# Kernel optimization log

Hardware: AMD Instinct MI355X
Metric: run time of the kernel (lower is better)

Reference implementation:

```python
import jax, jax.numpy as jnp
import numpy as np

B, L, S = 32, 8192, 128  # E == S == D == 128 required by the einsum labeling

def setup_inputs() -> dict:
    key = jax.random.key(0)
    kq, kk, kv = jax.random.split(key, 3)
    queries = jax.random.normal(kq, (B, L, S), dtype=jnp.float32)
    keys = jax.random.normal(kk, (B, S, S), dtype=jnp.float32)
    values = jax.random.normal(kv, (B, S, S), dtype=jnp.float32)
    return {"queries": queries, "keys": keys, "values": values}

def reference(queries, keys, values):
    # queries: (B, L, E), keys/values: (B, S, D) with E == S == D.
    # scores_1: sum-pooled outer product term (reduced-rank additive score)
    s1 = queries.sum(-1)[:, :, None] * keys.sum(-1)[:, None, :]   # (B, L, S)
    # scores_2: q contracted against key-position axis (plain batched matmul, no transpose)
    s2 = jnp.einsum('bls,bsd->bld', queries, keys)                # (B, L, S)
    A = jax.nn.softmax(s1 + s2, axis=-1)                          # (B, L, S)
    out = jnp.einsum('bls,bsd->bld', A, values)                   # (B, L, D)
    # original returns shape (B, 1, L, D) for the 3D-input path
    return out[:, None, :, :]
```

## Files before the change

kernel.cpp:

```cpp
#include <hip/hip_runtime.h>

#define SDIM 128
#define LDIM 8192
#define BATCH 32

#define WS_BATCH_BYTES 98304

typedef __attribute__((ext_vector_type(8))) short short8;
typedef __attribute__((ext_vector_type(16))) float float16;

union S8U { short8 v; unsigned short u[8]; unsigned w[4]; };
union FU { float f; unsigned u; };

static __device__ __forceinline__ unsigned short f2bf(float x) {
    FU v; v.f = x;
    unsigned r = v.u + 0x7fffu + ((v.u >> 16) & 1u);
    return (unsigned short)(r >> 16);
}
static __device__ __forceinline__ float bf2f(unsigned short h) {
    FU v; v.u = ((unsigned)h) << 16; return v.f;
}
static __device__ __forceinline__ float16 mfma_bf16(short8 a, short8 b, float16 c) {
    return __builtin_amdgcn_mfma_f32_32x32x16_bf16(a, b, c, 0, 0, 0);
}

__global__ __launch_bounds__(256) void prep_kernel(
        const float* __restrict__ keys, const float* __restrict__ values,
        char* __restrict__ ws) {
    __shared__ float T[SDIM * SDIM];
    __shared__ float ksum_s[SDIM];
    const int blk = blockIdx.x;
    const int b = blk >> 2;
    const int which = (blk >> 1) & 1;
    const int half = blk & 1;
    const int tid = threadIdx.x;
    const float* src = (which ? values : keys) + (size_t)b * SDIM * SDIM;

    #pragma unroll
    for (int it = 0; it < 16; ++it) {
        int i = tid + it * 256;
        int r = i >> 5, c0 = (i & 31) * 4;
        float4 v = ((const float4*)src)[i];
        float f[4] = {v.x, v.y, v.z, v.w};
        #pragma unroll
        for (int k = 0; k < 4; ++k)
            T[r * SDIM + ((c0 + k + r) & 127)] = f[k];
    }
    __syncthreads();

    if (which == 0) {
        int row = tid >> 1, hf = tid & 1;
        float s = 0.f;
        #pragma unroll
        for (int i = 0; i < 64; ++i) s += T[row * SDIM + hf * 64 + i];
        s += __shfl_xor(s, 1, 64);
        if (hf == 0) ksum_s[row] = s;
    }
    __syncthreads();

    char* dst = ws + (size_t)b * WS_BATCH_BYTES + (which ? 65536 : 0);
    #pragma unroll
    for (int it = 0; it < 4; ++it) {
        int entry = half * 1024 + it * 256 + tid;
        int m = entry >> 9;
        int ks = (entry >> 6) & 7;
        int lane = entry & 63;
        int ln = lane & 31, H = lane >> 5;
        int r = 32 * m + ln;
        int c0 = 16 * ks + 8 * H;
        if (which == 0) {
            float add = ksum_s[r];
            S8U hi, lo;
            #pragma unroll
            for (int i = 0; i < 8; ++i) {
                int e = c0 + i;
                float x = T[e * SDIM + ((r + e) & 127)] + add;
                unsigned short h = f2bf(x);
                hi.u[i] = h;
                lo.u[i] = f2bf(x - bf2f(h));
            }
            *(short8*)(dst + entry * 16) = hi.v;
            *(short8*)(dst + 32768 + entry * 16) = lo.v;
        } else {
            S8U hv;
            #pragma unroll
            for (int i = 0; i < 8; ++i) {
                int j = c0 + i;
                hv.u[i] = f2bf(T[j * SDIM + ((r + j) & 127)]);
            }
            *(short8*)(dst + entry * 16) = hv.v;
        }
    }
}

__global__ __launch_bounds__(256, 2) void attn_kernel(
        const float* __restrict__ q, const char* __restrict__ ws,
        float* __restrict__ out) {
    __shared__ char smQ[65536];
    const int blk = blockIdx.x;
    const int b = blk >> 6, tile = blk & 63;
    const int tid = threadIdx.x, wave = tid >> 6, lane = tid & 63;
    const int H = lane >> 5, ln = lane & 31;

    const char* wsb = ws + (size_t)b * WS_BATCH_BYTES;
    const float* qblk = q + ((size_t)b * LDIM + tile * 128) * SDIM;
    float* ob = out + ((size_t)b * LDIM + tile * 128 + wave * 32) * SDIM;

    {
        float4 buf[8][2];
        #pragma unroll
        for (int it = 0; it < 8; ++it) {
            int idx = it * 256 + tid;
            const float* p = qblk + (idx >> 4) * SDIM + (idx & 15) * 8;
            buf[it][0] = *(const float4*)p;
            buf[it][1] = *(const float4*)(p + 4);
        }
        #pragma unroll
        for (int it = 0; it < 8; ++it) {
            int idx = it * 256 + tid;
            int row = idx >> 4, cc = idx & 15;
            float f[8] = {buf[it][0].x, buf[it][0].y, buf[it][0].z, buf[it][0].w,
                          buf[it][1].x, buf[it][1].y, buf[it][1].z, buf[it][1].w};
            unsigned hiw[4], low[4];
            #pragma unroll
            for (int pr = 0; pr < 4; ++pr) {
                FU u0, u1; u0.f = f[2 * pr]; u1.f = f[2 * pr + 1];
                unsigned r0 = u0.u + 0x7fffu + ((u0.u >> 16) & 1u);
                unsigned r1 = u1.u + 0x7fffu + ((u1.u >> 16) & 1u);
                hiw[pr] = (r0 >> 16) | (r1 & 0xffff0000u);
                FU h0, h1; h0.u = r0 & 0xffff0000u; h1.u = r1 & 0xffff0000u;
                FU l0, l1; l0.f = f[2 * pr] - h0.f; l1.f = f[2 * pr + 1] - h1.f;
                low[pr] = (l0.u >> 16) | (l1.u & 0xffff0000u);
            }
            int off = row * 256 + ((cc ^ (row & 15)) * 16);
            *(uint4*)(smQ + off) = make_uint4(hiw[0], hiw[1], hiw[2], hiw[3]);
            *(uint4*)(smQ + 32768 + off) = make_uint4(low[0], low[1], low[2], low[3]);
        }
    }
    __syncthreads();

    const char* qrp = smQ + (wave * 32 + ln) * 256;
    const char* kph = wsb;
    const char* kpl = wsb + 32768;
    const char* vtf = wsb + 65536;
    const int lo16 = lane * 16;

    float16 acc[4];
    #pragma unroll
    for (int m = 0; m < 4; ++m) acc[m] = (float16)(0.0f);

    short8 ah[2][4], al[2][4];
    #pragma unroll
    for (int m = 0; m < 4; ++m) {
        ah[0][m] = *(const short8*)(kph + (m * 8) * 1024 + lo16);
        al[0][m] = *(const short8*)(kpl + (m * 8) * 1024 + lo16);
    }
    #pragma unroll
    for (int ks = 0; ks < 8; ++ks) {
        const int cur = ks & 1, nxt = cur ^ 1;
        if (ks < 7) {
            #pragma unroll
            for (int m = 0; m < 4; ++m) {
                ah[nxt][m] = *(const short8*)(kph + (m * 8 + ks + 1) * 1024 + lo16);
                al[nxt][m] = *(const short8*)(kpl + (m * 8 + ks + 1) * 1024 + lo16);
            }
        }
        int slot = ((2 * ks + H) ^ (ln & 15)) * 16;
        short8 bh = *(const short8*)(qrp + slot);
        short8 bl = *(const short8*)(qrp + 32768 + slot);
        #pragma unroll
        for (int m = 0; m < 4; ++m) acc[m] = mfma_bf16(ah[cur][m], bh, acc[m]);
        #pragma unroll
        for (int m = 0; m < 4; ++m) acc[m] = mfma_bf16(ah[cur][m], bl, acc[m]);
        #pragma unroll
        for (int m = 0; m < 4; ++m) acc[m] = mfma_bf16(al[cur][m], bh, acc[m]);
    }

    short8 av[2][4];
    #pragma unroll
    for (int dm = 0; dm < 4; ++dm)
        av[0][dm] = *(const short8*)(vtf + (dm * 8) * 1024 + lo16);

    float mx = -1e30f;
    #pragma unroll
    for (int m = 0; m < 4; ++m)
        #pragma unroll
        for (int r = 0; r < 16; ++r) mx = fmaxf(mx, acc[m][r]);
    mx = fmaxf(mx, __shfl_xor(mx, 32, 64));
    float sum = 0.0f;
    #pragma unroll
    for (int m = 0; m < 4; ++m)
        #pragma unroll
        for (int r = 0; r < 16; ++r) {
            float e = __expf(acc[m][r] - mx);
            acc[m][r] = e;
            sum += e;
        }
    sum += __shfl_xor(sum, 32, 64);
    const float inv = 1.0f / sum;

    unsigned pk[4][8];
    #pragma unroll
    for (int m = 0; m < 4; ++m)
        #pragma unroll
        for (int rr = 0; rr < 8; ++rr)
            pk[m][rr] = (unsigned)f2bf(acc[m][2 * rr] * inv) |
                        ((unsigned)f2bf(acc[m][2 * rr + 1] * inv) << 16);

    float16 oacc[4];
    #pragma unroll
    for (int m = 0; m < 4; ++m) oacc[m] = (float16)(0.0f);

    #pragma unroll
    for (int t = 0; t < 8; ++t) {
        const int cur = t & 1, nxt = cur ^ 1;
        if (t < 7) {
            #pragma unroll
            for (int dm = 0; dm < 4; ++dm)
                av[nxt][dm] = *(const short8*)(vtf + (dm * 8 + t + 1) * 1024 + lo16);
        }
        const int m = t >> 1;
        const int c = 4 * (t & 1);
        unsigned p0 = pk[m][c], p1 = pk[m][c + 1], p2 = pk[m][c + 2], p3 = pk[m][c + 3];
        unsigned a0 = H ? p2 : p0, a1 = H ? p3 : p1;
        unsigned s0 = H ? p0 : p2, s1 = H ? p1 : p3;
        unsigned r0 = (unsigned)__shfl_xor((int)s0, 32, 64);
        unsigned r1 = (unsigned)__shfl_xor((int)s1, 32, 64);
        S8U bf;
        bf.w[0] = H ? r0 : a0;
        bf.w[1] = H ? r1 : a1;
        bf.w[2] = H ? a0 : r0;
        bf.w[3] = H ? a1 : r1;
        #pragma unroll
        for (int dm = 0; dm < 4; ++dm)
            oacc[dm] = mfma_bf16(av[cur][dm], bf.v, oacc[dm]);
    }

    #pragma unroll
    for (int dm = 0; dm < 4; ++dm)
        #pragma unroll
        for (int g = 0; g < 4; ++g) {
            float4 v = make_float4(oacc[dm][4 * g], oacc[dm][4 * g + 1],
                                   oacc[dm][4 * g + 2], oacc[dm][4 * g + 3]);
            *(float4*)(ob + ln * SDIM + dm * 32 + g * 8 + H * 4) = v;
        }
}

extern "C" void kernel_launch(void* const* d_in, const int* in_sizes, int n_in,
                              void* d_out, int out_size, void* d_ws, size_t ws_size,
                              hipStream_t stream) {
    const float* q    = (const float*)d_in[0];
    const float* keys = (const float*)d_in[1];
    const float* vals = (const float*)d_in[2];
    float* out = (float*)d_out;
    char*  ws  = (char*)d_ws;

    prep_kernel<<<BATCH * 4, 256, 0, stream>>>(keys, vals, ws);
    attn_kernel<<<BATCH * (LDIM / 128), 256, 0, stream>>>(q, ws, out);
}
```

Before: 275.1 us.

## Switch to fp16 single-pass MFMA and apply rank-one sum term exactly in fp32

Replaces the bf16 hi/lo split (three MFMAs per step) with a single fp16 MFMA pass for Q·K and P·V. The rank-one qsum·ksum term is no longer folded into the keys. It is added in fp32 after the matmul, using row sums of Q computed on the fly and key sums written by the prep kernel. This cuts MFMA work and halves shared memory, so the launch bound rises to 4 blocks per CU. The risk is fp16 range and precision loss on the score matmul.

```diff
diff --git a/kernel.cpp b/kernel.cpp
--- a/kernel.cpp
+++ b/kernel.cpp
@@ -4,35 +4,25 @@
 #define LDIM 8192
 #define BATCH 32
 
-#define WS_BATCH_BYTES 98304
-
-typedef __attribute__((ext_vector_type(8))) short short8;
+#define WS_KV_STRIDE 65536
+#define WS_KSUM_OFF (BATCH * WS_KV_STRIDE)
+
+typedef __attribute__((ext_vector_type(8))) _Float16 half8;
 typedef __attribute__((ext_vector_type(16))) float float16;
 
-union S8U { short8 v; unsigned short u[8]; unsigned w[4]; };
-union FU { float f; unsigned u; };
-
-static __device__ __forceinline__ unsigned short f2bf(float x) {
-    FU v; v.f = x;
-    unsigned r = v.u + 0x7fffu + ((v.u >> 16) & 1u);
-    return (unsigned short)(r >> 16);
-}
-static __device__ __forceinline__ float bf2f(unsigned short h) {
-    FU v; v.u = ((unsigned)h) << 16; return v.f;
-}
-static __device__ __forceinline__ float16 mfma_bf16(short8 a, short8 b, float16 c) {
-    return __builtin_amdgcn_mfma_f32_32x32x16_bf16(a, b, c, 0, 0, 0);
+union H8U { half8 v; _Float16 h[8]; unsigned w[4]; };
+union PU { _Float16 h[2]; unsigned u; };
+
+static __device__ __forceinline__ float16 mfma_f16(half8 a, half8 b, float16 c) {
+    return __builtin_amdgcn_mfma_f32_32x32x16_f16(a, b, c, 0, 0, 0);
 }
 
 __global__ __launch_bounds__(256) void prep_kernel(
         const float* __restrict__ keys, const float* __restrict__ values,
         char* __restrict__ ws) {
     __shared__ float T[SDIM * SDIM];
-    __shared__ float ksum_s[SDIM];
-    const int blk = blockIdx.x;
-    const int b = blk >> 2;
-    const int which = (blk >> 1) & 1;
-    const int half = blk & 1;
+    const int b = blockIdx.x >> 1;
+    const int which = blockIdx.x & 1;
     const int tid = threadIdx.x;
     const float* src = (which ? values : keys) + (size_t)b * SDIM * SDIM;
 
@@ -48,138 +38,133 @@
     }
     __syncthreads();
 
-    if (which == 0) {
-        int row = tid >> 1, hf = tid & 1;
+    if (which == 0 && tid < SDIM) {
+        const float4* row = (const float4*)&T[tid * SDIM];
         float s = 0.f;
         #pragma unroll
-        for (int i = 0; i < 64; ++i) s += T[row * SDIM + hf * 64 + i];
-        s += __shfl_xor(s, 1, 64);
-        if (hf == 0) ksum_s[row] = s;
-    }
-    __syncthreads();
-
-    char* dst = ws + (size_t)b * WS_BATCH_BYTES + (which ? 65536 : 0);
-    #pragma unroll
-    for (int it = 0; it < 4; ++it) {
-        int entry = half * 1024 + it * 256 + tid;
-        int m = entry >> 9;
-        int ks = (entry >> 6) & 7;
-        int lane = entry & 63;
-        int ln = lane & 31, H = lane >> 5;
+        for (int i = 0; i < 32; ++i) { float4 v = row[i]; s += v.x + v.y + v.z + v.w; }
+        ((float*)(ws + WS_KSUM_OFF + b * 512))[tid] = s;
+    }
+
+    char* dst = ws + (size_t)b * WS_KV_STRIDE + (which ? 32768 : 0);
+    #pragma unroll
+    for (int it = 0; it < 8; ++it) {
+        int entry = it * 256 + tid;
+        int lane = entry & 63, ln = lane & 31, H = lane >> 5;
+        int m = entry >> 9, ks = (entry >> 6) & 7;
         int r = 32 * m + ln;
         int c0 = 16 * ks + 8 * H;
-        if (which == 0) {
-            float add = ksum_s[r];
-            S8U hi, lo;
-            #pragma unroll
-            for (int i = 0; i < 8; ++i) {
-                int e = c0 + i;
-                float x = T[e * SDIM + ((r + e) & 127)] + add;
-                unsigned short h = f2bf(x);
-                hi.u[i] = h;
-                lo.u[i] = f2bf(x - bf2f(h));
-            }
-            *(short8*)(dst + entry * 16) = hi.v;
-            *(short8*)(dst + 32768 + entry * 16) = lo.v;
-        } else {
-            S8U hv;
-            #pragma unroll
-            for (int i = 0; i < 8; ++i) {
-                int j = c0 + i;
-                hv.u[i] = f2bf(T[j * SDIM + ((r + j) & 127)]);
-            }
-            *(short8*)(dst + entry * 16) = hv.v;
-        }
-    }
-}
-
-__global__ __launch_bounds__(256, 2) void attn_kernel(
+        H8U o;
+        #pragma unroll
+        for (int i = 0; i < 8; ++i) {
+            int c = c0 + i;
+            o.h[i] = (_Float16)T[c * SDIM + ((r + c) & 127)];
+        }
+        *(half8*)(dst + entry * 16) = o.v;
+    }
+}
+
+__global__ __launch_bounds__(256, 4) void attn_kernel(
         const float* __restrict__ q, const char* __restrict__ ws,
         float* __restrict__ out) {
-    __shared__ char smQ[65536];
+    __shared__ char smQ[32768];
+    __shared__ float qsum_s[SDIM];
+    __shared__ float ksum_s[SDIM];
     const int blk = blockIdx.x;
     const int b = blk >> 6, tile = blk & 63;
     const int tid = threadIdx.x, wave = tid >> 6, lane = tid & 63;
     const int H = lane >> 5, ln = lane & 31;
 
-    const char* wsb = ws + (size_t)b * WS_BATCH_BYTES;
+    const char* wsb = ws + (size_t)b * WS_KV_STRIDE;
     const float* qblk = q + ((size_t)b * LDIM + tile * 128) * SDIM;
     float* ob = out + ((size_t)b * LDIM + tile * 128 + wave * 32) * SDIM;
 
+    if (tid < 32)
+        ((float4*)ksum_s)[tid] = ((const float4*)(ws + WS_KSUM_OFF + b * 512))[tid];
+
     {
-        float4 buf[8][2];
-        #pragma unroll
-        for (int it = 0; it < 8; ++it) {
+        float4 bufA[4][2], bufB[4][2];
+        #pragma unroll
+        for (int it = 0; it < 4; ++it) {
             int idx = it * 256 + tid;
             const float* p = qblk + (idx >> 4) * SDIM + (idx & 15) * 8;
-            buf[it][0] = *(const float4*)p;
-            buf[it][1] = *(const float4*)(p + 4);
-        }
-        #pragma unroll
-        for (int it = 0; it < 8; ++it) {
-            int idx = it * 256 + tid;
-            int row = idx >> 4, cc = idx & 15;
-            float f[8] = {buf[it][0].x, buf[it][0].y, buf[it][0].z, buf[it][0].w,
-                          buf[it][1].x, buf[it][1].y, buf[it][1].z, buf[it][1].w};
-            unsigned hiw[4], low[4];
+            bufA[it][0] = *(const float4*)p;
+            bufA[it][1] = *(const float4*)(p + 4);
+        }
+        #pragma unroll
+        for (int it = 0; it < 4; ++it) {
+            int idx = (it + 4) * 256 + tid;
+            const float* p = qblk + (idx >> 4) * SDIM + (idx & 15) * 8;
+            bufB[it][0] = *(const float4*)p;
+            bufB[it][1] = *(const float4*)(p + 4);
+        }
+        #pragma unroll
+        for (int g = 0; g < 2; ++g) {
             #pragma unroll
-            for (int pr = 0; pr < 4; ++pr) {
-                FU u0, u1; u0.f = f[2 * pr]; u1.f = f[2 * pr + 1];
-                unsigned r0 = u0.u + 0x7fffu + ((u0.u >> 16) & 1u);
-                unsigned r1 = u1.u + 0x7fffu + ((u1.u >> 16) & 1u);
-                hiw[pr] = (r0 >> 16) | (r1 & 0xffff0000u);
-                FU h0, h1; h0.u = r0 & 0xffff0000u; h1.u = r1 & 0xffff0000u;
-                FU l0, l1; l0.f = f[2 * pr] - h0.f; l1.f = f[2 * pr + 1] - h1.f;
-                low[pr] = (l0.u >> 16) | (l1.u & 0xffff0000u);
+            for (int it2 = 0; it2 < 4; ++it2) {
+                int it = g * 4 + it2;
+                int idx = it * 256 + tid;
+                int row = idx >> 4, cc = idx & 15;
+                float4 v0 = g ? bufB[it2][0] : bufA[it2][0];
+                float4 v1 = g ? bufB[it2][1] : bufA[it2][1];
+                float f[8] = {v0.x, v0.y, v0.z, v0.w, v1.x, v1.y, v1.z, v1.w};
+                float s = f[0] + f[1] + f[2] + f[3] + f[4] + f[5] + f[6] + f[7];
+                s += __shfl_xor(s, 1, 64);
+                s += __shfl_xor(s, 2, 64);
+                s += __shfl_xor(s, 4, 64);
+                s += __shfl_xor(s, 8, 64);
+                if ((tid & 15) == 0) qsum_s[row] = s;
+                H8U hv;
+                #pragma unroll
+                for (int i = 0; i < 8; ++i) hv.h[i] = (_Float16)f[i];
+                *(half8*)(smQ + row * 256 + ((cc ^ (row & 15)) * 16)) = hv.v;
             }
-            int off = row * 256 + ((cc ^ (row & 15)) * 16);
-            *(uint4*)(smQ + off) = make_uint4(hiw[0], hiw[1], hiw[2], hiw[3]);
-            *(uint4*)(smQ + 32768 + off) = make_uint4(low[0], low[1], low[2], low[3]);
         }
     }
     __syncthreads();
 
     const char* qrp = smQ + (wave * 32 + ln) * 256;
-    const char* kph = wsb;
-    const char* kpl = wsb + 32768;
-    const char* vtf = wsb + 65536;
+    const char* ktp = wsb;
+    const char* vtp = wsb + 32768;
     const int lo16 = lane * 16;
 
     float16 acc[4];
     #pragma unroll
     for (int m = 0; m < 4; ++m) acc[m] = (float16)(0.0f);
 
-    short8 ah[2][4], al[2][4];
-    #pragma unroll
-    for (int m = 0; m < 4; ++m) {
-        ah[0][m] = *(const short8*)(kph + (m * 8) * 1024 + lo16);
-        al[0][m] = *(const short8*)(kpl + (m * 8) * 1024 + lo16);
-    }
+    half8 ah[2][4];
+    #pragma unroll
+    for (int m = 0; m < 4; ++m)
+        ah[0][m] = *(const half8*)(ktp + (m * 8) * 1024 + lo16);
     #pragma unroll
     for (int ks = 0; ks < 8; ++ks) {
         const int cur = ks & 1, nxt = cur ^ 1;
         if (ks < 7) {
             #pragma unroll
-            for (int m = 0; m < 4; ++m) {
-                ah[nxt][m] = *(const short8*)(kph + (m * 8 + ks + 1) * 1024 + lo16);
-                al[nxt][m] = *(const short8*)(kpl + (m * 8 + ks + 1) * 1024 + lo16);
-            }
-        }
-        int slot = ((2 * ks + H) ^ (ln & 15)) * 16;
-        short8 bh = *(const short8*)(qrp + slot);
-        short8 bl = *(const short8*)(qrp + 32768 + slot);
-        #pragma unroll
-        for (int m = 0; m < 4; ++m) acc[m] = mfma_bf16(ah[cur][m], bh, acc[m]);
-        #pragma unroll
-        for (int m = 0; m < 4; ++m) acc[m] = mfma_bf16(ah[cur][m], bl, acc[m]);
-        #pragma unroll
-        for (int m = 0; m < 4; ++m) acc[m] = mfma_bf16(al[cur][m], bh, acc[m]);
-    }
-
-    short8 av[2][4];
+            for (int m = 0; m < 4; ++m)
+                ah[nxt][m] = *(const half8*)(ktp + (m * 8 + ks + 1) * 1024 + lo16);
+        }
+        half8 bh = *(const half8*)(qrp + ((2 * ks + H) ^ (ln & 15)) * 16);
+        #pragma unroll
+        for (int m = 0; m < 4; ++m) acc[m] = mfma_f16(ah[cur][m], bh, acc[m]);
+    }
+
+    half8 av[2][4];
     #pragma unroll
     for (int dm = 0; dm < 4; ++dm)
-        av[0][dm] = *(const short8*)(vtf + (dm * 8) * 1024 + lo16);
+        av[0][dm] = *(const half8*)(vtp + (dm * 8) * 1024 + lo16);
+
+    const float qs = qsum_s[wave * 32 + ln];
+    #pragma unroll
+    for (int m = 0; m < 4; ++m)
+        #pragma unroll
+        for (int g = 0; g < 4; ++g) {
+            float4 k4 = *(const float4*)&ksum_s[m * 32 + g * 8 + H * 4];
+            acc[m][4 * g + 0] = fmaf(k4.x, qs, acc[m][4 * g + 0]);
+            acc[m][4 * g + 1] = fmaf(k4.y, qs, acc[m][4 * g + 1]);
+            acc[m][4 * g + 2] = fmaf(k4.z, qs, acc[m][4 * g + 2]);
+            acc[m][4 * g + 3] = fmaf(k4.w, qs, acc[m][4 * g + 3]);
+        }
 
     float mx = -1e30f;
     #pragma unroll
@@ -203,9 +188,12 @@
     #pragma unroll
     for (int m = 0; m < 4; ++m)
         #pragma unroll
-        for (int rr = 0; rr < 8; ++rr)
-            pk[m][rr] = (unsigned)f2bf(acc[m][2 * rr] * inv) |
-                        ((unsigned)f2bf(acc[m][2 * rr + 1] * inv) << 16);
+        for (int rr = 0; rr < 8; ++rr) {
+            PU pu;
+            pu.h[0] = (_Float16)(acc[m][2 * rr] * inv);
+            pu.h[1] = (_Float16)(acc[m][2 * rr + 1] * inv);
+            pk[m][rr] = pu.u;
+        }
 
     float16 oacc[4];
     #pragma unroll
@@ -217,7 +205,7 @@
         if (t < 7) {
             #pragma unroll
             for (int dm = 0; dm < 4; ++dm)
-                av[nxt][dm] = *(const short8*)(vtf + (dm * 8 + t + 1) * 1024 + lo16);
+                av[nxt][dm] = *(const half8*)(vtp + (dm * 8 + t + 1) * 1024 + lo16);
         }
         const int m = t >> 1;
         const int c = 4 * (t & 1);
@@ -226,14 +214,14 @@
         unsigned s0 = H ? p0 : p2, s1 = H ? p1 : p3;
         unsigned r0 = (unsigned)__shfl_xor((int)s0, 32, 64);
         unsigned r1 = (unsigned)__shfl_xor((int)s1, 32, 64);
-        S8U bf;
+        H8U bf;
         bf.w[0] = H ? r0 : a0;
         bf.w[1] = H ? r1 : a1;
         bf.w[2] = H ? a0 : r0;
         bf.w[3] = H ? a1 : r1;
         #pragma unroll
         for (int dm = 0; dm < 4; ++dm)
-            oacc[dm] = mfma_bf16(av[cur][dm], bf.v, oacc[dm]);
+            oacc[dm] = mfma_f16(av[cur][dm], bf.v, oacc[dm]);
     }
 
     #pragma unroll
@@ -255,6 +243,6 @@
     float* out = (float*)d_out;
     char*  ws  = (char*)d_ws;
 
-    prep_kernel<<<BATCH * 4, 256, 0, stream>>>(keys, vals, ws);
+    prep_kernel<<<BATCH * 2, 256, 0, stream>>>(keys, vals, ws);
     attn_kernel<<<BATCH * (LDIM / 128), 256, 0, stream>>>(q, ws, out);
 }
```

After: 267.6 us. 2.7% less time.
